# Kernel optimization log

Hardware: AMD Instinct MI355X
Metric: run time of the kernel (lower is better)

The kernel has to match this reference:

```python
import jax, jax.numpy as jnp
import numpy as np

B, S, D, H = 2, 2048, 1024, 16
DH = D // H  # 64


def setup_inputs() -> dict:
    key = jax.random.key(0)
    ks = jax.random.split(key, 10)
    inp = {
        "q": jax.random.normal(ks[0], (B, S, D), jnp.float32),
        "k": jax.random.normal(ks[1], (B, S, D), jnp.float32),
        "v": jax.random.normal(ks[2], (B, S, D), jnp.float32),
        "mask": jax.random.randint(ks[3], (B, S), 0, 2, jnp.int32),
        "Wq": jax.random.normal(ks[4], (D, D), jnp.float32) * 0.02,
        "bq": jnp.zeros((D,), jnp.float32),
        "Wk": jax.random.normal(ks[5], (D, D), jnp.float32) * 0.02,
        "bk": jnp.zeros((D,), jnp.float32),
        "Wv": jax.random.normal(ks[6], (D, D), jnp.float32) * 0.02,
        "bv": jnp.zeros((D,), jnp.float32),
    }
    return inp


def _split_heads(x):
    # [B, S, D] -> [B, H, S, DH]
    b, s, _ = x.shape
    return x.reshape(b, s, H, DH).transpose(0, 2, 1, 3)


def reference(q, k, v, mask, Wq, bq, Wk, bk, Wv, bv):
    qh = _split_heads(q @ Wq + bq)
    kh = _split_heads(k @ Wk + bk)
    vh = _split_heads(v @ Wv + bv)
    # NOTE: original scales by sqrt(hidden_size), not sqrt(head_dim)
    scores = jnp.einsum("bhqd,bhkd->bhqk", qh, kh) / jnp.sqrt(jnp.float32(D))
    m = mask.astype(jnp.float32)[:, None, None, :]  # [B,1,1,S_k]
    scores = scores + (-1e9) * (1.0 - m)
    weights = jax.nn.softmax(scores, axis=-1)
    out = jnp.einsum("bhqk,bhkd->bhqd", weights, vh)
    # concat heads: [B,H,S,DH] -> [B,S,D]
    return out.transpose(0, 2, 1, 3).reshape(q.shape[0], -1, D)
```

## Files before the change

### kernel.cpp

```cpp
#include <hip/hip_runtime.h>


#define B_ 2
#define S_ 2048
#define D_ 1024
#define H_ 16
#define DH_ 64
#define M_ (B_*S_)

#define WT_OFF  ((size_t)3*4194304)
#define XB_OFF  (WT_OFF + (size_t)3*1048576)

typedef __attribute__((ext_vector_type(8))) short short8;
typedef __attribute__((ext_vector_type(4))) float f32x4;
typedef __attribute__((ext_vector_type(4))) unsigned int u32x4;
#define MFMA16(a,b,c) __builtin_amdgcn_mfma_f32_16x16x32_bf16(a,b,c,0,0,0)

typedef __attribute__((address_space(1))) const void* gptr_t;
typedef __attribute__((address_space(3))) void* lptr_t;
static __device__ inline void gload_lds16(const void* g, void* l) {
    __builtin_amdgcn_global_load_lds((gptr_t)g, (lptr_t)l, 16, 0, 0);
}

static __device__ inline unsigned short f2bf(float x) {
    union { float f; unsigned u; } v; v.f = x;
    return (unsigned short)((v.u + 0x7fffu + ((v.u >> 16) & 1u)) >> 16);
}
static __device__ inline unsigned packp(float a, float b) {
    return __builtin_amdgcn_perm(__float_as_uint(b) + 0x8000u,
                                 __float_as_uint(a) + 0x8000u, 0x07060302u);
}
static __device__ inline unsigned cvtpk(float a, float b) {
    unsigned r;
    asm("v_cvt_pk_bf16_f32 %0, %1, %2" : "=v"(r) : "v"(a), "v"(b));
    return r;
}

__global__ __launch_bounds__(256) void convert_all(
    const float* __restrict__ X0, const float* __restrict__ X1,
    const float* __restrict__ X2,
    const float* __restrict__ Wq, const float* __restrict__ Wk,
    const float* __restrict__ Wv,
    unsigned short* __restrict__ O0, unsigned short* __restrict__ O1,
    unsigned short* __restrict__ O2, unsigned short* __restrict__ WtBase)
{
    __shared__ unsigned short T[64][72];
    const int z = blockIdx.z;
    const int t = threadIdx.x;

    if (blockIdx.x < 2048) {
        const float* X = z==0 ? X0 : (z==1 ? X1 : X2);
        unsigned short* O = z==0 ? O0 : (z==1 ? O1 : O2);
        size_t e = ((size_t)(blockIdx.x*256 + t))*8;
        float4 a = *(const float4*)&X[e];
        float4 b = *(const float4*)&X[e+4];
        uint4 o;
        o.x = (unsigned)f2bf(a.x) | ((unsigned)f2bf(a.y) << 16);
        o.y = (unsigned)f2bf(a.z) | ((unsigned)f2bf(a.w) << 16);
        o.z = (unsigned)f2bf(b.x) | ((unsigned)f2bf(b.y) << 16);
        o.w = (unsigned)f2bf(b.z) | ((unsigned)f2bf(b.w) << 16);
        *(uint4*)&O[e] = o;
        return;
    }

    const float* W = z==0 ? Wq : (z==1 ? Wk : Wv);
    unsigned short* Out = WtBase + ((size_t)z << 20);
    const int bx2 = blockIdx.x - 2048;
    const int n0 = (bx2 & 15)*64, k0 = (bx2 >> 4)*64;
    const int tk = t >> 4, tn4 = (t & 15)*4;

    #pragma unroll
    for (int i=0;i<4;i++){
        int kk = tk + i*16;
        float4 wv = *(const float4*)&W[(size_t)(k0+kk)*D_ + n0 + tn4];
        T[tn4+0][kk] = f2bf(wv.x);
        T[tn4+1][kk] = f2bf(wv.y);
        T[tn4+2][kk] = f2bf(wv.z);
        T[tn4+3][kk] = f2bf(wv.w);
    }
    __syncthreads();

    const int n = t >> 2, seg = t & 3;
    uint4 a = *(uint4*)&T[n][seg*16];
    uint4 b = *(uint4*)&T[n][seg*16 + 8];
    *(uint4*)&Out[(size_t)(n0+n)*D_ + k0 + seg*16]     = a;
    *(uint4*)&Out[(size_t)(n0+n)*D_ + k0 + seg*16 + 8] = b;
}

__global__ __launch_bounds__(256) void proj_gemm(
    const unsigned short* __restrict__ A0, const unsigned short* __restrict__ A1,
    const unsigned short* __restrict__ A2, const unsigned short* __restrict__ WtBase,
    const float* __restrict__ b0, const float* __restrict__ b1,
    const float* __restrict__ b2, unsigned short* __restrict__ OutBase)
{
    const int lin0 = blockIdx.x + (blockIdx.y << 3) + (blockIdx.z << 8);
    const int swz  = (lin0 & 7)*96 + (lin0 >> 3);
    const int bxn  = swz & 7;
    const int byn  = (swz >> 3) & 31;
    const int which = swz >> 8;

    const unsigned short* A  = which==0 ? A0 : (which==1 ? A1 : A2);
    const unsigned short* Bm = WtBase + ((size_t)which << 20);
    const float* bias        = which==0 ? b0 : (which==1 ? b1 : b2);
    unsigned short* Out      = OutBase + ((size_t)which << 22);
    const float oscale = (which==0) ? 0.04508422f : 1.0f;

    __shared__ __align__(16) unsigned short As[2*128*64];
    __shared__ __align__(16) unsigned short Bs[2*128*64];

    const int t    = threadIdx.x;
    const int m0   = byn * 128;
    const int n0   = bxn * 128;
    const int w    = t >> 6;
    const int lane = t & 63;
    const int l15  = lane & 15;
    const int quad = lane >> 4;
    const int wm   = w >> 1, wn = w & 1;

    f32x4 acc[4][4];
    #pragma unroll
    for (int i=0;i<4;i++)
        #pragma unroll
        for (int j=0;j<4;j++) acc[i][j] = (f32x4){0.f,0.f,0.f,0.f};

    float biasv[4];
    #pragma unroll
    for (int nt=0; nt<4; nt++)
        biasv[nt] = bias[n0 + wn*64 + nt*16 + l15];

    int sArow[4], sAkc[4];
    #pragma unroll
    for (int i=0;i<4;i++){
        int s  = (w*4 + i)*64 + lane;
        int r  = s >> 3, cs = s & 7;
        sArow[i] = r;
        sAkc[i]  = ((cs ^ (r & 7)) * 8);
    }

    #define PISSUE(ksv, buf) do {                                              \
        const int kb = (ksv)*64;                                               \
        _Pragma("unroll")                                                      \
        for (int i=0;i<4;i++){                                                 \
            int s = (w*4 + i)*64 + lane;                                       \
            gload_lds16(A  + (size_t)(m0 + sArow[i])*D_ + kb + sAkc[i],        \
                        (unsigned short*)As + (buf)*8192 + s*8);               \
            gload_lds16(Bm + (size_t)(n0 + sArow[i])*D_ + kb + sAkc[i],        \
                        (unsigned short*)Bs + (buf)*8192 + s*8);               \
        }                                                                      \
    } while(0)

    PISSUE(0, 0);
    int cur = 0;
    for (int ks = 0; ks < 16; ++ks) {
        if (ks < 15) {
            PISSUE(ks+1, cur^1);
            asm volatile("s_waitcnt vmcnt(8)" ::: "memory");
        } else {
            asm volatile("s_waitcnt vmcnt(0)" ::: "memory");
        }
        __builtin_amdgcn_s_barrier();
        __builtin_amdgcn_sched_barrier(0);

        const unsigned short* Asb = As + cur*8192;
        const unsigned short* Bsb = Bs + cur*8192;
        #pragma unroll
        for (int kh=0; kh<2; kh++){
            short8 aF[4], bF[4];
            #pragma unroll
            for (int mt=0; mt<4; mt++){
                int r  = wm*64 + mt*16 + l15;
                int cs = (kh*4 + quad) ^ (r & 7);
                aF[mt] = *(const short8*)(Asb + r*64 + cs*8);
            }
            #pragma unroll
            for (int nt=0; nt<4; nt++){
                int r  = wn*64 + nt*16 + l15;
                int cs = (kh*4 + quad) ^ (r & 7);
                bF[nt] = *(const short8*)(Bsb + r*64 + cs*8);
            }
            #pragma unroll
            for (int mt=0; mt<4; mt++)
                #pragma unroll
                for (int nt=0; nt<4; nt++)
                    acc[mt][nt] = MFMA16(aF[mt], bF[nt], acc[mt][nt]);
        }
        __builtin_amdgcn_s_barrier();
        cur ^= 1;
    }

    if (which != 2) {
        #pragma unroll
        for (int nt=0; nt<4; nt++){
            int n  = n0 + wn*64 + nt*16 + l15;
            int hh = n >> 6, dh = n & 63;
            #pragma unroll
            for (int mt=0; mt<4; mt++){
                #pragma unroll
                for (int r=0; r<4; r++){
                    int m  = m0 + wm*64 + mt*16 + quad*4 + r;
                    int bb = m >> 11, ss = m & (S_-1);
                    float v = (acc[mt][nt][r] + biasv[nt]) * oscale;
                    Out[((size_t)((bb*H_ + hh)*S_ + ss))*DH_ + dh] = f2bf(v);
                }
            }
        }
    } else {
        #pragma unroll
        for (int nt=0; nt<4; nt++){
            int n  = n0 + wn*64 + nt*16 + l15;
            int hh = n >> 6, dh = n & 63;
            #pragma unroll
            for (int mt=0; mt<4; mt++){
                int m  = m0 + wm*64 + mt*16 + quad*4;
                int bb = m >> 11, ss = m & (S_-1);
                uint2 pk;
                pk.x = packp(acc[mt][nt][0] + biasv[nt], acc[mt][nt][1] + biasv[nt]);
                pk.y = packp(acc[mt][nt][2] + biasv[nt], acc[mt][nt][3] + biasv[nt]);
                *(uint2*)&Out[((size_t)((bb*H_ + hh)*DH_ + dh))*S_ + ss] = pk;
            }
        }
    }
    #undef PISSUE
}

__global__ __launch_bounds__(512, 2) void attn_kernel(
    const unsigned short* __restrict__ ws, const int* __restrict__ mask,
    float* __restrict__ out)
{
    const unsigned short* Qh = ws;
    const unsigned short* Kh = ws + (size_t)M_*D_;
    const unsigned short* Vg = ws + 2*(size_t)M_*D_;

    const int lin = blockIdx.x + (blockIdx.y << 3) + (blockIdx.z << 7);
    const int Wn  = (lin & 7)*32 + (lin >> 3);
    const int qt = Wn & 7;
    const int h  = (Wn >> 3) & 15;
    const int bb = Wn >> 7;

    const size_t base = ((size_t)(bb*H_ + h)) * S_ * DH_;
    const int q0 = qt * 256;

    __shared__ __align__(16) unsigned char smem[73728];
    unsigned short* KsB = (unsigned short*)smem;
    unsigned short* VtB = (unsigned short*)(smem + 32768);
    float*          MsT = (float*)(smem + 65536);
    float*          Ob  = (float*)smem;

    const int t    = threadIdx.x;
    const int w    = t >> 6;
    const int lane = t & 63;
    const int l15  = lane & 15;
    const int quad = lane >> 4;

    short8 qf[2][2];
    #pragma unroll
    for (int qs=0; qs<2; qs++){
        const unsigned short* qp = Qh + base + (size_t)(q0 + w*32 + qs*16 + l15)*DH_ + quad*8;
        qf[qs][0] = *(const short8*)(qp);
        qf[qs][1] = *(const short8*)(qp + 32);
    }

    f32x4 accO[2][4];
    #pragma unroll
    for (int qs=0; qs<2; qs++)
        #pragma unroll
        for (int i=0;i<4;i++) accO[qs][i] = (f32x4){0.f,0.f,0.f,0.f};
    f32x4 lv[2] = {(f32x4){0.f,0.f,0.f,0.f}, (f32x4){0.f,0.f,0.f,0.f}};

    int rr[2], cc[2], ssl[2], gK[2];
    #pragma unroll
    for (int i=0;i<2;i++){
        int s  = (w*2 + i)*64 + lane;
        int r  = s >> 3, cs = s & 7;
        int r6 = r & 63;
        ssl[i] = s;
        rr[i]  = r;
        cc[i]  = (cs ^ (r & 7)) * 8;
        gK[i]  = (r & 64) + ((r6 >> 4) & 1)*32 + ((r6 >> 2) & 3)*8 + (r6 >> 5)*4 + (r6 & 3);
    }

    #define ISSUE128(k0v, p) do {                                              \
        _Pragma("unroll")                                                      \
        for (int i=0;i<2;i++){                                                 \
            gload_lds16(Kh + base + (size_t)((k0v) + gK[i])*DH_ + cc[i],       \
                        KsB + (p)*8192 + ssl[i]*8);                            \
            gload_lds16(Vg + base + (size_t)(rr[i] & 63)*S_ + (k0v)            \
                            + (rr[i] & 64) + cc[i],                            \
                        VtB + (p)*8192 + ssl[i]*8);                            \
        }                                                                      \
    } while(0)

    ISSUE128(0, 0);
    #pragma unroll
    for (int i=0;i<4;i++){
        int idx = i*512 + t;
        MsT[idx] = mask[bb*S_ + idx] ? 0.f : -1e9f;
    }
    __syncthreads();

    for (int it = 0; it < 16; ++it){
        const int p = it & 1;
        if (it < 15) ISSUE128((it+1)*128, 1-p);

        #pragma unroll
        for (int sbi = 0; sbi < 2; ++sbi){
            const int sb = sbi ^ (w & 1);
            const unsigned short* Ks  = KsB + p*8192 + sb*4096;
            const unsigned short* Vts = VtB + p*8192 + sb*4096;
            const float*          Mp  = MsT + it*128 + sb*64;

            f32x4 msv[4];
            #pragma unroll
            for (int st=0; st<4; st++)
                msv[st] = *(const f32x4*)&Mp[(st&1)*32 + (st>>1)*4 + quad*8];

            short8 ka[4], kb[4];
            #pragma unroll
            for (int st=0; st<4; st++){
                int row = st*16 + l15;
                const unsigned short* kr = Ks + row*64;
                ka[st] = *(const short8*)(kr + ((quad    ) ^ (row & 7))*8);
                kb[st] = *(const short8*)(kr + ((quad + 4) ^ (row & 7))*8);
            }
            short8 vf[4][2];
            #pragma unroll
            for (int mt=0; mt<4; mt++){
                int row = mt*16 + l15;
                const unsigned short* vr = Vts + row*64;
                vf[mt][0] = *(const short8*)(vr + ((quad    ) ^ (row & 7))*8);
                vf[mt][1] = *(const short8*)(vr + ((quad + 4) ^ (row & 7))*8);
            }

            #pragma unroll
            for (int qs=0; qs<2; qs++){
                f32x4 sc[4];
                __builtin_amdgcn_s_setprio(1);
                #pragma unroll
                for (int st=0; st<4; st++){
                    f32x4 a = msv[st];
                    a = MFMA16(ka[st], qf[qs][0], a);
                    a = MFMA16(kb[st], qf[qs][1], a);
                    sc[st] = a;
                }
                __builtin_amdgcn_s_setprio(0);
                f32x4 pvv[4];
                #pragma unroll
                for (int st=0; st<4; st++)
                    #pragma unroll
                    for (int rj=0; rj<4; rj++)
                        pvv[st][rj] = __builtin_amdgcn_exp2f(sc[st][rj]);
                f32x4 s01 = pvv[0] + pvv[1];
                f32x4 s23 = pvv[2] + pvv[3];
                lv[qs] += (s01 + s23);
                u32x4 u0 = { cvtpk(pvv[0][0],pvv[0][1]), cvtpk(pvv[0][2],pvv[0][3]),
                             cvtpk(pvv[2][0],pvv[2][1]), cvtpk(pvv[2][2],pvv[2][3]) };
                u32x4 u1 = { cvtpk(pvv[1][0],pvv[1][1]), cvtpk(pvv[1][2],pvv[1][3]),
                             cvtpk(pvv[3][0],pvv[3][1]), cvtpk(pvv[3][2],pvv[3][3]) };
                short8 pf0 = __builtin_bit_cast(short8, u0);
                short8 pf1 = __builtin_bit_cast(short8, u1);
                __builtin_amdgcn_s_setprio(1);
                #pragma unroll
                for (int mt=0; mt<4; mt++){
                    accO[qs][mt] = MFMA16(vf[mt][0], pf0, accO[qs][mt]);
                    accO[qs][mt] = MFMA16(vf[mt][1], pf1, accO[qs][mt]);
                }
                __builtin_amdgcn_s_setprio(0);
            }
        }
        __syncthreads();
    }

    #pragma unroll
    for (int qs=0; qs<2; qs++){
        float l = (lv[qs][0] + lv[qs][1]) + (lv[qs][2] + lv[qs][3]);
        l += __shfl_xor(l, 16);
        l += __shfl_xor(l, 32);
        float invl = 1.0f / fmaxf(l, 1e-30f);
        #pragma unroll
        for (int mt=0; mt<4; mt++)
            #pragma unroll
            for (int r=0; r<4; r++)
                Ob[(w*32 + qs*16 + l15)*68 + mt*16 + quad*4 + r] = accO[qs][mt][r]*invl;
    }
    __syncthreads();

    #pragma unroll
    for (int i=0;i<8;i++){
        int f  = (i*512 + t)*4;
        int qq = f >> 6, dh = f & 63;
        float4 o = *(float4*)&Ob[qq*68 + dh];
        *(float4*)&out[((size_t)(bb*S_ + q0 + qq))*D_ + h*DH_ + dh] = o;
    }
    #undef ISSUE128
}

extern "C" void kernel_launch(void* const* d_in, const int* in_sizes, int n_in,
                              void* d_out, int out_size, void* d_ws, size_t ws_size,
                              hipStream_t stream) {
    const float* q    = (const float*)d_in[0];
    const float* k    = (const float*)d_in[1];
    const float* v    = (const float*)d_in[2];
    const int*   mask = (const int*)d_in[3];
    const float* Wq   = (const float*)d_in[4];
    const float* b0   = (const float*)d_in[5];
    const float* Wk   = (const float*)d_in[6];
    const float* b1   = (const float*)d_in[7];
    const float* Wv   = (const float*)d_in[8];
    const float* b2   = (const float*)d_in[9];
    float* out = (float*)d_out;
    unsigned short* ws = (unsigned short*)d_ws;

    unsigned short* xq = ws + XB_OFF;
    unsigned short* xk = (unsigned short*)d_out;
    unsigned short* xv = (unsigned short*)d_out + 4194304;

    convert_all<<<dim3(2304,1,3), 256, 0, stream>>>(q, k, v, Wq, Wk, Wv,
                                                    xq, xk, xv, ws + WT_OFF);
    proj_gemm<<<dim3(8,32,3), 256, 0, stream>>>(xq, xk, xv, ws + WT_OFF,
                                                b0, b1, b2, ws);
    attn_kernel<<<dim3(8,16,2), 512, 0, stream>>>(ws, mask, out);
}
```

Before: 190.3 us.

## Make projection GEMM persistent with 64x128 tiles and XCD-aware scheduling

The QKV projection GEMM now uses 64x128 output tiles instead of 128x128. It launches 512 blocks, and each block loops over three tiles chosen so that consecutive tiles stay on the same XCD. The goal is to remove the tail imbalance of the old 768-block grid of large tiles on 256 CUs and to improve L2 locality. In exchange, each wave does fewer MFMAs per LDS load, which lowers arithmetic intensity, and the per-tile loop is serialized inside each block.

```diff
diff --git a/kernel.cpp b/kernel.cpp
--- a/kernel.cpp
+++ b/kernel.cpp
@@ -93,130 +93,139 @@
     const float* __restrict__ b0, const float* __restrict__ b1,
     const float* __restrict__ b2, unsigned short* __restrict__ OutBase)
 {
-    const int lin0 = blockIdx.x + (blockIdx.y << 3) + (blockIdx.z << 8);
-    const int swz  = (lin0 & 7)*96 + (lin0 >> 3);
-    const int bxn  = swz & 7;
-    const int byn  = (swz >> 3) & 31;
-    const int which = swz >> 8;
-
-    const unsigned short* A  = which==0 ? A0 : (which==1 ? A1 : A2);
-    const unsigned short* Bm = WtBase + ((size_t)which << 20);
-    const float* bias        = which==0 ? b0 : (which==1 ? b1 : b2);
-    unsigned short* Out      = OutBase + ((size_t)which << 22);
-    const float oscale = (which==0) ? 0.04508422f : 1.0f;
-
-    __shared__ __align__(16) unsigned short As[2*128*64];
+    const int blk  = blockIdx.x;
+    const int xcd  = blk & 7;
+    const int slot = blk >> 3;
+
+    __shared__ __align__(16) unsigned short As[2*64*64];
     __shared__ __align__(16) unsigned short Bs[2*128*64];
 
     const int t    = threadIdx.x;
-    const int m0   = byn * 128;
-    const int n0   = bxn * 128;
     const int w    = t >> 6;
     const int lane = t & 63;
     const int l15  = lane & 15;
     const int quad = lane >> 4;
-    const int wm   = w >> 1, wn = w & 1;
-
-    f32x4 acc[4][4];
-    #pragma unroll
-    for (int i=0;i<4;i++)
-        #pragma unroll
-        for (int j=0;j<4;j++) acc[i][j] = (f32x4){0.f,0.f,0.f,0.f};
-
-    float biasv[4];
-    #pragma unroll
-    for (int nt=0; nt<4; nt++)
-        biasv[nt] = bias[n0 + wn*64 + nt*16 + l15];
-
-    int sArow[4], sAkc[4];
+
+    int aR[2], aC[2], aS[2];
+    #pragma unroll
+    for (int i=0;i<2;i++){
+        int s = (w*2 + i)*64 + lane;
+        int r = s >> 3, cs = s & 7;
+        aS[i] = s; aR[i] = r; aC[i] = ((cs ^ (r & 7)) * 8);
+    }
+    int bR[4], bC[4], bS[4];
     #pragma unroll
     for (int i=0;i<4;i++){
-        int s  = (w*4 + i)*64 + lane;
-        int r  = s >> 3, cs = s & 7;
-        sArow[i] = r;
-        sAkc[i]  = ((cs ^ (r & 7)) * 8);
+        int s = (w*4 + i)*64 + lane;
+        int r = s >> 3, cs = s & 7;
+        bS[i] = s; bR[i] = r; bC[i] = ((cs ^ (r & 7)) * 8);
     }
 
     #define PISSUE(ksv, buf) do {                                              \
         const int kb = (ksv)*64;                                               \
         _Pragma("unroll")                                                      \
-        for (int i=0;i<4;i++){                                                 \
-            int s = (w*4 + i)*64 + lane;                                       \
-            gload_lds16(A  + (size_t)(m0 + sArow[i])*D_ + kb + sAkc[i],        \
-                        (unsigned short*)As + (buf)*8192 + s*8);               \
-            gload_lds16(Bm + (size_t)(n0 + sArow[i])*D_ + kb + sAkc[i],        \
-                        (unsigned short*)Bs + (buf)*8192 + s*8);               \
-        }                                                                      \
+        for (int i=0;i<2;i++)                                                  \
+            gload_lds16(A  + (size_t)(m0 + aR[i])*D_ + kb + aC[i],             \
+                        (unsigned short*)As + (buf)*4096 + aS[i]*8);           \
+        _Pragma("unroll")                                                      \
+        for (int i=0;i<4;i++)                                                  \
+            gload_lds16(Bm + (size_t)(n0 + bR[i])*D_ + kb + bC[i],             \
+                        (unsigned short*)Bs + (buf)*8192 + bS[i]*8);           \
     } while(0)
 
-    PISSUE(0, 0);
-    int cur = 0;
-    for (int ks = 0; ks < 16; ++ks) {
-        if (ks < 15) {
-            PISSUE(ks+1, cur^1);
-            asm volatile("s_waitcnt vmcnt(8)" ::: "memory");
+    for (int j = 0; j < 3; ++j){
+        const int tid = xcd*192 + slot + j*64;
+        const int zm  = tid >> 3, nn = tid & 7;
+        const int which = zm >> 6, tm = zm & 63;
+        const int m0 = tm * 64;
+        const int n0 = nn * 128;
+
+        const unsigned short* A  = which==0 ? A0 : (which==1 ? A1 : A2);
+        const unsigned short* Bm = WtBase + ((size_t)which << 20);
+        const float* bias        = which==0 ? b0 : (which==1 ? b1 : b2);
+        unsigned short* Out      = OutBase + ((size_t)which << 22);
+        const float oscale = (which==0) ? 0.04508422f : 1.0f;
+
+        float biasv[2];
+        #pragma unroll
+        for (int nt=0; nt<2; nt++)
+            biasv[nt] = bias[n0 + w*32 + nt*16 + l15];
+
+        f32x4 acc[4][2];
+        #pragma unroll
+        for (int i=0;i<4;i++)
+            #pragma unroll
+            for (int jj=0;jj<2;jj++) acc[i][jj] = (f32x4){0.f,0.f,0.f,0.f};
+
+        PISSUE(0, 0);
+        int cur = 0;
+        for (int ks = 0; ks < 16; ++ks) {
+            if (ks < 15) {
+                PISSUE(ks+1, cur^1);
+                asm volatile("s_waitcnt vmcnt(6)" ::: "memory");
+            } else {
+                asm volatile("s_waitcnt vmcnt(0)" ::: "memory");
+            }
+            __builtin_amdgcn_s_barrier();
+            __builtin_amdgcn_sched_barrier(0);
+
+            const unsigned short* Asb = As + cur*4096;
+            const unsigned short* Bsb = Bs + cur*8192;
+            #pragma unroll
+            for (int kh=0; kh<2; kh++){
+                short8 aF[4], bF[2];
+                #pragma unroll
+                for (int mt=0; mt<4; mt++){
+                    int r  = mt*16 + l15;
+                    int cs = (kh*4 + quad) ^ (r & 7);
+                    aF[mt] = *(const short8*)(Asb + r*64 + cs*8);
+                }
+                #pragma unroll
+                for (int nt=0; nt<2; nt++){
+                    int r  = w*32 + nt*16 + l15;
+                    int cs = (kh*4 + quad) ^ (r & 7);
+                    bF[nt] = *(const short8*)(Bsb + r*64 + cs*8);
+                }
+                #pragma unroll
+                for (int mt=0; mt<4; mt++)
+                    #pragma unroll
+                    for (int nt=0; nt<2; nt++)
+                        acc[mt][nt] = MFMA16(aF[mt], bF[nt], acc[mt][nt]);
+            }
+            __builtin_amdgcn_s_barrier();
+            cur ^= 1;
+        }
+
+        if (which != 2) {
+            #pragma unroll
+            for (int nt=0; nt<2; nt++){
+                int n  = n0 + w*32 + nt*16 + l15;
+                int hh = n >> 6, dh = n & 63;
+                #pragma unroll
+                for (int mt=0; mt<4; mt++){
+                    #pragma unroll
+                    for (int r=0; r<4; r++){
+                        int m  = m0 + mt*16 + quad*4 + r;
+                        int bb = m >> 11, ss = m & (S_-1);
+                        float v = (acc[mt][nt][r] + biasv[nt]) * oscale;
+                        Out[((size_t)((bb*H_ + hh)*S_ + ss))*DH_ + dh] = f2bf(v);
+                    }
+                }
+            }
         } else {
-            asm volatile("s_waitcnt vmcnt(0)" ::: "memory");
-        }
-        __builtin_amdgcn_s_barrier();
-        __builtin_amdgcn_sched_barrier(0);
-
-        const unsigned short* Asb = As + cur*8192;
-        const unsigned short* Bsb = Bs + cur*8192;
-        #pragma unroll
-        for (int kh=0; kh<2; kh++){
-            short8 aF[4], bF[4];
-            #pragma unroll
-            for (int mt=0; mt<4; mt++){
-                int r  = wm*64 + mt*16 + l15;
-                int cs = (kh*4 + quad) ^ (r & 7);
-                aF[mt] = *(const short8*)(Asb + r*64 + cs*8);
-            }
-            #pragma unroll
-            for (int nt=0; nt<4; nt++){
-                int r  = wn*64 + nt*16 + l15;
-                int cs = (kh*4 + quad) ^ (r & 7);
-                bF[nt] = *(const short8*)(Bsb + r*64 + cs*8);
-            }
-            #pragma unroll
-            for (int mt=0; mt<4; mt++)
-                #pragma unroll
-                for (int nt=0; nt<4; nt++)
-                    acc[mt][nt] = MFMA16(aF[mt], bF[nt], acc[mt][nt]);
-        }
-        __builtin_amdgcn_s_barrier();
-        cur ^= 1;
-    }
-
-    if (which != 2) {
-        #pragma unroll
-        for (int nt=0; nt<4; nt++){
-            int n  = n0 + wn*64 + nt*16 + l15;
-            int hh = n >> 6, dh = n & 63;
-            #pragma unroll
-            for (int mt=0; mt<4; mt++){
-                #pragma unroll
-                for (int r=0; r<4; r++){
-                    int m  = m0 + wm*64 + mt*16 + quad*4 + r;
+            #pragma unroll
+            for (int nt=0; nt<2; nt++){
+                int n  = n0 + w*32 + nt*16 + l15;
+                int hh = n >> 6, dh = n & 63;
+                #pragma unroll
+                for (int mt=0; mt<4; mt++){
+                    int m  = m0 + mt*16 + quad*4;
                     int bb = m >> 11, ss = m & (S_-1);
-                    float v = (acc[mt][nt][r] + biasv[nt]) * oscale;
-                    Out[((size_t)((bb*H_ + hh)*S_ + ss))*DH_ + dh] = f2bf(v);
-                }
-            }
-        }
-    } else {
-        #pragma unroll
-        for (int nt=0; nt<4; nt++){
-            int n  = n0 + wn*64 + nt*16 + l15;
-            int hh = n >> 6, dh = n & 63;
-            #pragma unroll
-            for (int mt=0; mt<4; mt++){
-                int m  = m0 + wm*64 + mt*16 + quad*4;
-                int bb = m >> 11, ss = m & (S_-1);
-                uint2 pk;
-                pk.x = packp(acc[mt][nt][0] + biasv[nt], acc[mt][nt][1] + biasv[nt]);
-                pk.y = packp(acc[mt][nt][2] + biasv[nt], acc[mt][nt][3] + biasv[nt]);
-                *(uint2*)&Out[((size_t)((bb*H_ + hh)*DH_ + dh))*S_ + ss] = pk;
+                    uint2 pk;
+                    pk.x = packp(acc[mt][nt][0] + biasv[nt], acc[mt][nt][1] + biasv[nt]);
+                    pk.y = packp(acc[mt][nt][2] + biasv[nt], acc[mt][nt][3] + biasv[nt]);
+                    *(uint2*)&Out[((size_t)((bb*H_ + hh)*DH_ + dh))*S_ + ss] = pk;
+                }
             }
         }
     }
@@ -416,7 +425,7 @@
 
     convert_all<<<dim3(2304,1,3), 256, 0, stream>>>(q, k, v, Wq, Wk, Wv,
                                                     xq, xk, xv, ws + WT_OFF);
-    proj_gemm<<<dim3(8,32,3), 256, 0, stream>>>(xq, xk, xv, ws + WT_OFF,
-                                                b0, b1, b2, ws);
+    proj_gemm<<<dim3(512,1,1), 256, 0, stream>>>(xq, xk, xv, ws + WT_OFF,
+                                                 b0, b1, b2, ws);
     attn_kernel<<<dim3(8,16,2), 512, 0, stream>>>(ws, mask, out);
 }
```

Measured after the change: 188.3 us. Within noise of the previous version (-1.0%).
